# Kernel optimization log

Measured on AMD Instinct MI355X. Metric: run time of the kernel, lower is better.

The kernel has to match this reference:

```python
import jax, jax.numpy as jnp
import numpy as np

N = 50000

def gcn_conv(x, W, b, src, dst, n_nodes):
    # PyG GCNConv: h = x @ W; add self-loops; sym-normalize; scatter-add; + bias
    h = x @ W  # [N, d_out]
    loop = jnp.arange(n_nodes, dtype=src.dtype)
    s = jnp.concatenate([src, loop])
    d = jnp.concatenate([dst, loop])
    deg = jax.ops.segment_sum(jnp.ones_like(d, dtype=h.dtype), d, num_segments=n_nodes)
    dinv = jnp.where(deg > 0, jax.lax.rsqrt(deg), 0.0)
    norm = dinv[s] * dinv[d]  # [E+N]
    msgs = h[s] * norm[:, None]  # gather + scale
    out = jax.ops.segment_sum(msgs, d, num_segments=n_nodes)  # scatter-add
    return out + b

def setup_inputs() -> dict:
    key = jax.random.key(0)
    k1, k2, k3, k4 = jax.random.split(key, 4)
    in_c, hid_c, out_c, E = 512, 256, 64, 800000
    x = jax.random.normal(k1, (N, in_c), dtype=jnp.float32)
    edge_index = jax.random.randint(k2, (2, E), 0, N, dtype=jnp.int64)
    W1 = jax.random.normal(k3, (in_c, hid_c), dtype=jnp.float32) / np.sqrt(in_c)
    b1 = jnp.zeros((hid_c,), dtype=jnp.float32)
    W2 = jax.random.normal(k4, (hid_c, out_c), dtype=jnp.float32) / np.sqrt(hid_c)
    b2 = jnp.zeros((out_c,), dtype=jnp.float32)
    return {"x": x, "edge_index": edge_index, "W1": W1, "b1": b1, "W2": W2, "b2": b2}

def reference(x, edge_index, W1, b1, W2, b2):
    src, dst = edge_index[0], edge_index[1]
    h = gcn_conv(x, W1, b1, src, dst, N)
    h = jax.nn.relu(h)
    h = gcn_conv(h, W2, b2, src, dst, N)
    return jax.nn.log_softmax(h, axis=1)
```

## Files before the change

### kernel.cpp

```cpp
#include <hip/hip_runtime.h>
#include <hip/hip_bf16.h>

#define IN_C 512
#define HID_C 256
#define OUT_C 64

typedef __attribute__((ext_vector_type(8))) short bf16x8;
typedef __attribute__((ext_vector_type(4))) float f32x4;
typedef __attribute__((ext_vector_type(2))) float f32x2;

__device__ __forceinline__ ushort f2bf(float f) {
  __hip_bfloat16 h = __float2bfloat16(f);
  union { __hip_bfloat16 h; ushort u; } v; v.h = h; return v.u;
}
__device__ __forceinline__ uint pack2bf(float a, float b) {
  return (uint)f2bf(a) | ((uint)f2bf(b) << 16);
}
__device__ __forceinline__ float u2f(uint u) {
  union { uint i; float f; } v; v.i = u; return v.f;
}
__device__ __forceinline__ void pkacc(f32x2& aLo, f32x2& aHi, uint ux, uint uy) {
  f32x2 lo, hi;
  lo[0] = u2f(ux << 16);         lo[1] = u2f(uy << 16);
  hi[0] = u2f(ux & 0xffff0000u); hi[1] = u2f(uy & 0xffff0000u);
  aLo += lo;
  aHi += hi;
}
__device__ __forceinline__ void glds16(const ushort* g, ushort* l) {
  __builtin_amdgcn_global_load_lds(
      (const __attribute__((address_space(1))) unsigned int*)(const void*)g,
      (__attribute__((address_space(3))) unsigned int*)(void*)l, 16, 0, 0);
}


__global__ void deg_count_tw(const int* __restrict__ dst, int* __restrict__ counts, int E, int eb,
                             const float* __restrict__ W1, ushort* __restrict__ W1t,
                             const float* __restrict__ W2, ushort* __restrict__ W2t) {
  if ((int)blockIdx.x < eb) {
    int e = blockIdx.x * 256 + threadIdx.x;
    if (e < E) atomicAdd(&counts[dst[e]], 1);
    return;
  }
  int b2 = blockIdx.x - eb;
  int z = b2 >> 7;
  int rem = b2 & 127;
  int bx = rem & 7, by = rem >> 3;
  const float* W; ushort* Wt; int K, N;
  if (z == 0) { W = W1; Wt = W1t; K = IN_C; N = HID_C; }
  else        { W = W2; Wt = W2t; K = HID_C; N = OUT_C; }
  int n0 = bx * 32, k0 = by * 32;
  if (n0 >= N || k0 >= K) return;
  __shared__ ushort t[32][33];
  int tx = threadIdx.x & 31;
  int ty = threadIdx.x >> 5;
#pragma unroll
  for (int i = 0; i < 4; ++i) {
    int k = k0 + ty + i * 8;
    t[ty + i * 8][tx] = f2bf(W[(size_t)k * N + n0 + tx]);
  }
  __syncthreads();
#pragma unroll
  for (int i = 0; i < 4; ++i) {
    int n = n0 + ty + i * 8;
    Wt[(size_t)n * K + k0 + tx] = t[tx][ty + i * 8];
  }
}

#define SCAN_TILE 1024

__global__ __launch_bounds__(256) void scan_block_sums(const int* __restrict__ counts,
                                                       int* __restrict__ partial, int n) {
  int base = blockIdx.x * SCAN_TILE + threadIdx.x * 4;
  int s = 0;
  if (base + 3 < n) {
    int4 v = *(const int4*)(counts + base);
    s = v.x + v.y + v.z + v.w;
  } else {
#pragma unroll
    for (int i = 0; i < 4; ++i) if (base + i < n) s += counts[base + i];
  }
#pragma unroll
  for (int off = 1; off < 64; off <<= 1) s += __shfl_xor(s, off);
  __shared__ int ws[4];
  int lane = threadIdx.x & 63, wid = threadIdx.x >> 6;
  if (lane == 0) ws[wid] = s;
  __syncthreads();
  if (threadIdx.x == 0) partial[blockIdx.x] = ws[0] + ws[1] + ws[2] + ws[3];
}

__global__ __launch_bounds__(256) void scan_write(const int* __restrict__ counts,
                                                  const int* __restrict__ partial,
                                                  int* __restrict__ offs,
                                                  int* __restrict__ cur,
                                                  float* __restrict__ dinv,
                                                  int n, int E, int nb) {
  __shared__ int sbase;
  int tid = threadIdx.x;
  if (tid < 64) {
    int v = (tid < (int)blockIdx.x && tid < nb) ? partial[tid] : 0;
#pragma unroll
    for (int off = 1; off < 64; off <<= 1) v += __shfl_xor(v, off);
    if (tid == 0) sbase = v;
  }
  __syncthreads();
  int pbase = sbase;
  int base = blockIdx.x * SCAN_TILE + tid * 4;
  int4 c = make_int4(0, 0, 0, 0);
  if (base + 3 < n) {
    c = *(const int4*)(counts + base);
  } else {
    if (base + 0 < n) c.x = counts[base + 0];
    if (base + 1 < n) c.y = counts[base + 1];
    if (base + 2 < n) c.z = counts[base + 2];
  }
  int tsum = c.x + c.y + c.z + c.w;
  int lane = tid & 63, wid = tid >> 6;
  int incl = tsum;
#pragma unroll
  for (int off = 1; off < 64; off <<= 1) {
    int y = __shfl_up(incl, off);
    if (lane >= off) incl += y;
  }
  __shared__ int ws[4];
  if (lane == 63) ws[wid] = incl;
  __syncthreads();
  int wbase = 0;
#pragma unroll
  for (int w = 0; w < 4; ++w) if (w < wid) wbase += ws[w];
  int off0 = pbase + wbase + (incl - tsum);
  int4 ov;
  ov.x = off0;
  ov.y = off0 + c.x;
  ov.z = off0 + c.x + c.y;
  ov.w = off0 + c.x + c.y + c.z;
  float4 dv;
  dv.x = rsqrtf((float)(c.x + 1));
  dv.y = rsqrtf((float)(c.y + 1));
  dv.z = rsqrtf((float)(c.z + 1));
  dv.w = rsqrtf((float)(c.w + 1));
  if (base + 3 < n) {
    *(int4*)(offs + base) = ov;
    *(int4*)(cur + base) = ov;
    *(float4*)(dinv + base) = dv;
  } else {
    int o4[4] = {ov.x, ov.y, ov.z, ov.w};
    float d4[4] = {dv.x, dv.y, dv.z, dv.w};
    for (int i = 0; i < 4; ++i)
      if (base + i < n) { offs[base + i] = o4[i]; cur[base + i] = o4[i]; dinv[base + i] = d4[i]; }
  }
  if (blockIdx.x == 0 && tid == 0) offs[n] = E;
}

__global__ void fill_adj(const int* __restrict__ src, const int* __restrict__ dst,
                         int* __restrict__ cur, int* __restrict__ adj, int E) {
  int e = blockIdx.x * 256 + threadIdx.x;
  if (e >= E) return;
  int pos = atomicAdd(&cur[dst[e]], 1);
  adj[pos] = src[e];
}


__global__ __launch_bounds__(512) void gemm1_fs(const float* __restrict__ A,
                                                const ushort* __restrict__ Bt,
                                                const float* __restrict__ dinv,
                                                ushort* __restrict__ C, int M) {
  __shared__ __align__(16) ushort As[2][128 * 32];
  __shared__ __align__(16) ushort Bs[2][256 * 32];
  int tid = threadIdx.x;
  int lane = tid & 63, wid = tid >> 6;
  int m0 = blockIdx.x * 128;
  int arow = tid >> 2, acol = (tid & 3) * 8;
  int gma = m0 + arow; if (gma >= M) gma = M - 1;
  const float* gA = A + (size_t)gma * IN_C + acol;
  int rb0 = tid >> 2, cb0 = (tid & 3) * 8;
  int rb1 = (tid + 512) >> 2;
  const ushort* gB0 = Bt + (size_t)rb0 * IN_C + cb0;
  const ushort* gB1 = Bt + (size_t)rb1 * IN_C + cb0;

  int wr = wid >> 2, wc = wid & 3;
  int kf = (lane >> 4) * 8, rl = lane & 15;
  f32x4 acc[4][4] = {};

  {
    float4 p0 = *(const float4*)gA;
    float4 p1 = *(const float4*)(gA + 4);
    glds16(gB0, &Bs[0][tid * 8]);
    glds16(gB1, &Bs[0][(tid + 512) * 8]);
    uint4 w;
    w.x = pack2bf(p0.x, p0.y); w.y = pack2bf(p0.z, p0.w);
    w.z = pack2bf(p1.x, p1.y); w.w = pack2bf(p1.z, p1.w);
    *(uint4*)&As[0][arow * 32 + acol] = w;
  }
  __syncthreads();

  int cur = 0;
  for (int t = 0; t < 16; ++t) {
    float4 p0, p1;
    if (t < 15) {
      const float* g = gA + (t + 1) * 32;
      p0 = *(const float4*)g;
      p1 = *(const float4*)(g + 4);
      glds16(gB0 + (t + 1) * 32, &Bs[cur ^ 1][tid * 8]);
      glds16(gB1 + (t + 1) * 32, &Bs[cur ^ 1][(tid + 512) * 8]);
    }
    bf16x8 af[4], bf[4];
#pragma unroll
    for (int i = 0; i < 4; ++i)
      af[i] = *(const bf16x8*)&As[cur][(wr * 64 + i * 16 + rl) * 32 + kf];
#pragma unroll
    for (int j = 0; j < 4; ++j)
      bf[j] = *(const bf16x8*)&Bs[cur][(wc * 64 + j * 16 + rl) * 32 + kf];
#pragma unroll
    for (int i = 0; i < 4; ++i)
#pragma unroll
      for (int j = 0; j < 4; ++j)
        acc[i][j] = __builtin_amdgcn_mfma_f32_16x16x32_bf16(af[i], bf[j], acc[i][j], 0, 0, 0);
    if (t < 15) {
      uint4 w;
      w.x = pack2bf(p0.x, p0.y); w.y = pack2bf(p0.z, p0.w);
      w.z = pack2bf(p1.x, p1.y); w.w = pack2bf(p1.z, p1.w);
      *(uint4*)&As[cur ^ 1][arow * 32 + acol] = w;
    }
    __syncthreads();
    cur ^= 1;
  }

  int r4 = (lane >> 4) * 4;
  int cl = lane & 15;
#pragma unroll
  for (int i = 0; i < 4; ++i) {
#pragma unroll
    for (int r = 0; r < 4; ++r) {
      int gr = m0 + wr * 64 + i * 16 + r4 + r;
      if (gr < M) {
        float dv = dinv[gr];
#pragma unroll
        for (int j = 0; j < 4; ++j) {
          int gc = wc * 64 + j * 16 + cl;
          C[(size_t)gr * HID_C + gc] = f2bf(dv * acc[i][j][r]);
        }
      }
    }
  }
}

__global__ __launch_bounds__(256) void gemm2(const ushort* __restrict__ A,
                                             const ushort* __restrict__ Bt,
                                             const float* __restrict__ dinv,
                                             ushort* __restrict__ C, int M) {
  __shared__ __align__(16) ushort As[2][64 * 32];
  __shared__ __align__(16) ushort Bs[2][64 * 32];
  int tid = threadIdx.x;
  int lane = tid & 63, wid = tid >> 6;
  int m0 = blockIdx.x * 64;
  int arow = tid >> 2, acol = (tid & 3) * 8;
  int gma = m0 + arow; if (gma >= M) gma = M - 1;
  const ushort* gA = A + (size_t)gma * HID_C + acol;
  const ushort* gB = Bt + (size_t)arow * HID_C + acol;

  int wm = wid * 16;
  int kf = (lane >> 4) * 8, rl = lane & 15;
  f32x4 acc[4] = {};

  glds16(gA, &As[0][tid * 8]);
  glds16(gB, &Bs[0][tid * 8]);
  __syncthreads();

  int cur = 0;
  for (int t = 0; t < 8; ++t) {
    if (t < 7) {
      int k0 = (t + 1) * 32;
      glds16(gA + k0, &As[cur ^ 1][tid * 8]);
      glds16(gB + k0, &Bs[cur ^ 1][tid * 8]);
    }
    bf16x8 a, b[4];
    a = *(const bf16x8*)&As[cur][(wm + rl) * 32 + kf];
#pragma unroll
    for (int j = 0; j < 4; ++j)
      b[j] = *(const bf16x8*)&Bs[cur][(j * 16 + rl) * 32 + kf];
#pragma unroll
    for (int j = 0; j < 4; ++j)
      acc[j] = __builtin_amdgcn_mfma_f32_16x16x32_bf16(a, b[j], acc[j], 0, 0, 0);
    __syncthreads();
    cur ^= 1;
  }

  int r4 = (lane >> 4) * 4;
  int cl = lane & 15;
#pragma unroll
  for (int r = 0; r < 4; ++r) {
    int gr = m0 + wm + r4 + r;
    if (gr < M) {
      float dv = dinv[gr];
#pragma unroll
      for (int j = 0; j < 4; ++j) {
        int gc = j * 16 + cl;
        C[(size_t)gr * OUT_C + gc] = f2bf(dv * acc[j][r]);
      }
    }
  }
}


__global__ __launch_bounds__(256) void agg1(const ushort* __restrict__ h,
                                            ushort* __restrict__ out,
                                            const float* __restrict__ dinv,
                                            const int* __restrict__ offs,
                                            const int* __restrict__ adj,
                                            const float* __restrict__ bias, int Nn) {
  int node = blockIdx.x * 4 + (threadIdx.x >> 6);
  if (node >= Nn) return;
  int lane = threadIdx.x & 63;
  int slot = lane >> 4;
  int c0 = (lane & 15) * 16;
  int e0 = offs[node];
  int cnt = offs[node + 1] - e0 + 1;
  const ushort* hc = h + c0;
  f32x2 aLo[4] = {}, aHi[4] = {};
  for (int b0 = 0; b0 < cnt; b0 += 64) {
    int vk = b0 + lane;
    int myadj = node;
    if (vk > 0 && vk < cnt) myadj = adj[e0 + vk - 1];
    int bn = cnt - b0; if (bn > 64) bn = 64;
    int iters = (bn + 3) >> 2;
#pragma unroll 4
    for (int i = 0; i < iters; ++i) {
      int k = slot + 4 * i;
      int s = __shfl(myadj, k < bn ? k : 0);
      if (k < bn) {
        const uint4* rp = (const uint4*)(hc + (size_t)s * HID_C);
        uint4 u0 = rp[0];
        uint4 u1 = rp[1];
        pkacc(aLo[0], aHi[0], u0.x, u0.y);
        pkacc(aLo[1], aHi[1], u0.z, u0.w);
        pkacc(aLo[2], aHi[2], u1.x, u1.y);
        pkacc(aLo[3], aHi[3], u1.z, u1.w);
      }
    }
  }
  float r16[16];
#pragma unroll
  for (int q = 0; q < 4; ++q) {
    r16[4 * q + 0] = aLo[q][0];
    r16[4 * q + 1] = aHi[q][0];
    r16[4 * q + 2] = aLo[q][1];
    r16[4 * q + 3] = aHi[q][1];
  }
#pragma unroll
  for (int i = 0; i < 16; ++i) {
    r16[i] += __shfl_xor(r16[i], 16);
    r16[i] += __shfl_xor(r16[i], 32);
  }
  if (lane < 16) {
    float dv = dinv[node];
    const float4* bp = (const float4*)(bias + c0);
    float bb[16];
#pragma unroll
    for (int q = 0; q < 4; ++q) {
      float4 b4 = bp[q];
      bb[q * 4 + 0] = b4.x; bb[q * 4 + 1] = b4.y;
      bb[q * 4 + 2] = b4.z; bb[q * 4 + 3] = b4.w;
    }
    uint r[8];
#pragma unroll
    for (int i = 0; i < 8; ++i) {
      float v0 = fmaxf(dv * r16[2 * i]     + bb[2 * i],     0.f);
      float v1 = fmaxf(dv * r16[2 * i + 1] + bb[2 * i + 1], 0.f);
      r[i] = (uint)f2bf(v0) | ((uint)f2bf(v1) << 16);
    }
    uint4* op = (uint4*)(out + (size_t)node * HID_C + c0);
    op[0] = make_uint4(r[0], r[1], r[2], r[3]);
    op[1] = make_uint4(r[4], r[5], r[6], r[7]);
  }
}

__global__ __launch_bounds__(256) void agg2(const ushort* __restrict__ h,
                                            float* __restrict__ out,
                                            const float* __restrict__ dinv,
                                            const int* __restrict__ offs,
                                            const int* __restrict__ adj,
                                            const float* __restrict__ bias, int Nn) {
  int node = blockIdx.x * 4 + (threadIdx.x >> 6);
  if (node >= Nn) return;
  int lane = threadIdx.x & 63;
  int slot = lane >> 3;
  int c0 = (lane & 7) * 8;
  int e0 = offs[node];
  int cnt = offs[node + 1] - e0 + 1;
  const ushort* hc = h + c0;
  f32x2 aLo[2] = {}, aHi[2] = {};
  for (int b0 = 0; b0 < cnt; b0 += 64) {
    int vk = b0 + lane;
    int myadj = node;
    if (vk > 0 && vk < cnt) myadj = adj[e0 + vk - 1];
    int bn = cnt - b0; if (bn > 64) bn = 64;
    int iters = (bn + 7) >> 3;
#pragma unroll 4
    for (int i = 0; i < iters; ++i) {
      int k = slot + 8 * i;
      int s = __shfl(myadj, k < bn ? k : 0);
      if (k < bn) {
        uint4 u = *(const uint4*)(hc + (size_t)s * OUT_C);
        pkacc(aLo[0], aHi[0], u.x, u.y);
        pkacc(aLo[1], aHi[1], u.z, u.w);
      }
    }
  }
  float r8[8];
#pragma unroll
  for (int q = 0; q < 2; ++q) {
    r8[4 * q + 0] = aLo[q][0];
    r8[4 * q + 1] = aHi[q][0];
    r8[4 * q + 2] = aLo[q][1];
    r8[4 * q + 3] = aHi[q][1];
  }
#pragma unroll
  for (int i = 0; i < 8; ++i) {
    r8[i] += __shfl_xor(r8[i], 8);
    r8[i] += __shfl_xor(r8[i], 16);
    r8[i] += __shfl_xor(r8[i], 32);
  }
  float dv = dinv[node];
  const float4* bp = (const float4*)(bias + c0);
  float4 bb0 = bp[0], bb1 = bp[1];
  float v[8];
  v[0] = dv * r8[0] + bb0.x; v[1] = dv * r8[1] + bb0.y;
  v[2] = dv * r8[2] + bb0.z; v[3] = dv * r8[3] + bb0.w;
  v[4] = dv * r8[4] + bb1.x; v[5] = dv * r8[5] + bb1.y;
  v[6] = dv * r8[6] + bb1.z; v[7] = dv * r8[7] + bb1.w;
  float m = v[0];
#pragma unroll
  for (int i = 1; i < 8; ++i) m = fmaxf(m, v[i]);
  m = fmaxf(m, __shfl_xor(m, 1));
  m = fmaxf(m, __shfl_xor(m, 2));
  m = fmaxf(m, __shfl_xor(m, 4));
  float s8 = 0.f;
#pragma unroll
  for (int i = 0; i < 8; ++i) s8 += expf(v[i] - m);
  s8 += __shfl_xor(s8, 1);
  s8 += __shfl_xor(s8, 2);
  s8 += __shfl_xor(s8, 4);
  float lg = logf(s8);
  if (lane < 8) {
    float4* op = (float4*)(out + (size_t)node * OUT_C + c0);
    op[0] = make_float4(v[0] - m - lg, v[1] - m - lg, v[2] - m - lg, v[3] - m - lg);
    op[1] = make_float4(v[4] - m - lg, v[5] - m - lg, v[6] - m - lg, v[7] - m - lg);
  }
}


extern "C" void kernel_launch(void* const* d_in, const int* in_sizes, int n_in,
                              void* d_out, int out_size, void* d_ws, size_t ws_size,
                              hipStream_t stream) {
  const float* x  = (const float*)d_in[0];
  const int*   ei = (const int*)d_in[1];
  const float* W1 = (const float*)d_in[2];
  const float* b1 = (const float*)d_in[3];
  const float* W2 = (const float*)d_in[4];
  const float* b2 = (const float*)d_in[5];
  float* outp = (float*)d_out;

  int Nn = in_sizes[0] / IN_C;
  int E  = in_sizes[1] / 2;
  const int* srcv = ei;
  const int* dstv = ei + E;

  char* ws = (char*)d_ws;
  size_t o = 0;
  auto alloc = [&](size_t bytes) {
    char* p = ws + o;
    o = (o + bytes + 255) & ~(size_t)255;
    return p;
  };
  float*  dinv  = (float*)alloc((size_t)Nn * 4);
  int*    counts= (int*)alloc((size_t)Nn * 4);
  int*    offs  = (int*)alloc((size_t)(Nn + 1) * 4);
  int*    cur   = (int*)alloc((size_t)Nn * 4);
  int*    adj   = (int*)alloc((size_t)E * 4);
  int*    partial=(int*)alloc((size_t)((Nn + SCAN_TILE - 1) / SCAN_TILE) * 4);
  ushort* W1t   = (ushort*)alloc((size_t)IN_C * HID_C * 2);
  ushort* W2t   = (ushort*)alloc((size_t)HID_C * OUT_C * 2);
  ushort* h1p   = (ushort*)alloc((size_t)Nn * HID_C * 2);
  ushort* h1a   = (ushort*)alloc((size_t)Nn * HID_C * 2);
  ushort* h2p   = (ushort*)alloc((size_t)Nn * OUT_C * 2);

  int eb = (E + 255) / 256;
  int sb = (Nn + SCAN_TILE - 1) / SCAN_TILE;

  hipMemsetAsync(counts, 0, (size_t)Nn * 4, stream);
  deg_count_tw<<<eb + 256, 256, 0, stream>>>(dstv, counts, E, eb, W1, W1t, W2, W2t);
  scan_block_sums<<<sb, 256, 0, stream>>>(counts, partial, Nn);
  scan_write<<<sb, 256, 0, stream>>>(counts, partial, offs, cur, dinv, Nn, E, sb);
  fill_adj<<<eb, 256, 0, stream>>>(srcv, dstv, cur, adj, E);

  gemm1_fs<<<(Nn + 127) / 128, 512, 0, stream>>>(x, W1t, dinv, h1p, Nn);
  agg1<<<(Nn + 3) / 4, 256, 0, stream>>>(h1p, h1a, dinv, offs, adj, b1, Nn);
  gemm2<<<(Nn + 63) / 64, 256, 0, stream>>>(h1a, W2t, dinv, h2p, Nn);
  agg2<<<(Nn + 3) / 4, 256, 0, stream>>>(h2p, outp, dinv, offs, adj, b2, Nn);
}
```

Before: 226.5 us.

## Split layer-1 aggregation across eight feature slices per node

The first-layer aggregation kernel now processes each node's 256 features as eight 32-column slices, each in its own block, with 8 lanes per edge reading 8 bytes instead of 16 lanes reading 32 bytes. This gives 8x more blocks and more edges in flight per wave, and cuts the cross-lane reduction and register footprint. The cost is that adjacency and offsets are re-read once per slice, and each gathered row segment is only 64 bytes, which may use memory transactions less well. Adjacency loads are also marked nontemporal.

```diff
diff --git a/kernel.cpp b/kernel.cpp
--- a/kernel.cpp
+++ b/kernel.cpp
@@ -302,75 +302,56 @@
 }
 
 
-__global__ __launch_bounds__(256) void agg1(const ushort* __restrict__ h,
-                                            ushort* __restrict__ out,
-                                            const float* __restrict__ dinv,
-                                            const int* __restrict__ offs,
-                                            const int* __restrict__ adj,
-                                            const float* __restrict__ bias, int Nn) {
-  int node = blockIdx.x * 4 + (threadIdx.x >> 6);
+__global__ __launch_bounds__(256) void agg1s(const ushort* __restrict__ h,
+                                             ushort* __restrict__ out,
+                                             const float* __restrict__ dinv,
+                                             const int* __restrict__ offs,
+                                             const int* __restrict__ adj,
+                                             const float* __restrict__ bias, int Nn) {
+  int slice = blockIdx.x & 7;
+  int node = (blockIdx.x >> 3) * 4 + (threadIdx.x >> 6);
   if (node >= Nn) return;
   int lane = threadIdx.x & 63;
-  int slot = lane >> 4;
-  int c0 = (lane & 15) * 16;
+  int slot = lane >> 3;
+  int c0 = slice * 32 + (lane & 7) * 4;
   int e0 = offs[node];
   int cnt = offs[node + 1] - e0 + 1;
   const ushort* hc = h + c0;
-  f32x2 aLo[4] = {}, aHi[4] = {};
+  f32x2 aLo = {}, aHi = {};
   for (int b0 = 0; b0 < cnt; b0 += 64) {
     int vk = b0 + lane;
     int myadj = node;
-    if (vk > 0 && vk < cnt) myadj = adj[e0 + vk - 1];
+    if (vk > 0 && vk < cnt) myadj = __builtin_nontemporal_load(&adj[e0 + vk - 1]);
     int bn = cnt - b0; if (bn > 64) bn = 64;
-    int iters = (bn + 3) >> 2;
+    int iters = (bn + 7) >> 3;
 #pragma unroll 4
     for (int i = 0; i < iters; ++i) {
-      int k = slot + 4 * i;
+      int k = slot + 8 * i;
       int s = __shfl(myadj, k < bn ? k : 0);
       if (k < bn) {
-        const uint4* rp = (const uint4*)(hc + (size_t)s * HID_C);
-        uint4 u0 = rp[0];
-        uint4 u1 = rp[1];
-        pkacc(aLo[0], aHi[0], u0.x, u0.y);
-        pkacc(aLo[1], aHi[1], u0.z, u0.w);
-        pkacc(aLo[2], aHi[2], u1.x, u1.y);
-        pkacc(aLo[3], aHi[3], u1.z, u1.w);
+        uint2 u = *(const uint2*)(hc + (size_t)s * HID_C);
+        pkacc(aLo, aHi, u.x, u.y);
       }
     }
   }
-  float r16[16];
-#pragma unroll
-  for (int q = 0; q < 4; ++q) {
-    r16[4 * q + 0] = aLo[q][0];
-    r16[4 * q + 1] = aHi[q][0];
-    r16[4 * q + 2] = aLo[q][1];
-    r16[4 * q + 3] = aHi[q][1];
-  }
-#pragma unroll
-  for (int i = 0; i < 16; ++i) {
-    r16[i] += __shfl_xor(r16[i], 16);
-    r16[i] += __shfl_xor(r16[i], 32);
-  }
-  if (lane < 16) {
+  float r[4] = {aLo[0], aHi[0], aLo[1], aHi[1]};
+#pragma unroll
+  for (int i = 0; i < 4; ++i) {
+    r[i] += __shfl_xor(r[i], 8);
+    r[i] += __shfl_xor(r[i], 16);
+    r[i] += __shfl_xor(r[i], 32);
+  }
+  if (lane < 8) {
     float dv = dinv[node];
-    const float4* bp = (const float4*)(bias + c0);
-    float bb[16];
-#pragma unroll
-    for (int q = 0; q < 4; ++q) {
-      float4 b4 = bp[q];
-      bb[q * 4 + 0] = b4.x; bb[q * 4 + 1] = b4.y;
-      bb[q * 4 + 2] = b4.z; bb[q * 4 + 3] = b4.w;
-    }
-    uint r[8];
-#pragma unroll
-    for (int i = 0; i < 8; ++i) {
-      float v0 = fmaxf(dv * r16[2 * i]     + bb[2 * i],     0.f);
-      float v1 = fmaxf(dv * r16[2 * i + 1] + bb[2 * i + 1], 0.f);
-      r[i] = (uint)f2bf(v0) | ((uint)f2bf(v1) << 16);
-    }
-    uint4* op = (uint4*)(out + (size_t)node * HID_C + c0);
-    op[0] = make_uint4(r[0], r[1], r[2], r[3]);
-    op[1] = make_uint4(r[4], r[5], r[6], r[7]);
+    float4 bb = *(const float4*)(bias + c0);
+    float v0 = fmaxf(dv * r[0] + bb.x, 0.f);
+    float v1 = fmaxf(dv * r[1] + bb.y, 0.f);
+    float v2 = fmaxf(dv * r[2] + bb.z, 0.f);
+    float v3 = fmaxf(dv * r[3] + bb.w, 0.f);
+    uint2 p;
+    p.x = pack2bf(v0, v1);
+    p.y = pack2bf(v2, v3);
+    *(uint2*)(out + (size_t)node * HID_C + c0) = p;
   }
 }
 
@@ -494,7 +475,7 @@
   fill_adj<<<eb, 256, 0, stream>>>(srcv, dstv, cur, adj, E);
 
   gemm1_fs<<<(Nn + 127) / 128, 512, 0, stream>>>(x, W1t, dinv, h1p, Nn);
-  agg1<<<(Nn + 3) / 4, 256, 0, stream>>>(h1p, h1a, dinv, offs, adj, b1, Nn);
+  agg1s<<<((Nn + 3) / 4) * 8, 256, 0, stream>>>(h1p, h1a, dinv, offs, adj, b1, Nn);
   gemm2<<<(Nn + 63) / 64, 256, 0, stream>>>(h1a, W2t, dinv, h2p, Nn);
   agg2<<<(Nn + 3) / 4, 256, 0, stream>>>(h2p, outp, dinv, offs, adj, b2, Nn);
 }
```

Measured after the change: 322.2 us. +42.3%, slower.
